# Performance work log

Measured on AMD Instinct MI355X. Metric: run time of the kernel, lower is better.

Reference implementation:

```python
import jax, jax.numpy as jnp
import numpy as np

N = 50000
E = 640000
IN_DIM = 23
HID = 128
NUM_CLASS = 12


def setup_inputs() -> dict:
    key = jax.random.key(0)
    ks = jax.random.split(key, 12)
    x = jax.random.normal(ks[0], (N, IN_DIM), dtype=jnp.float32)
    edge_index = jax.random.randint(ks[1], (2, E), 0, N, dtype=jnp.int32)

    def glorot(k, shape):
        fan_in, fan_out = shape
        lim = np.sqrt(6.0 / (fan_in + fan_out)).astype(np.float32)
        return jax.random.uniform(k, shape, jnp.float32, -lim, lim)

    W1 = glorot(ks[2], (IN_DIM, HID)); b1 = jnp.zeros((HID,), jnp.float32)
    W2 = glorot(ks[3], (HID, HID));    b2 = jnp.zeros((HID,), jnp.float32)
    W3 = glorot(ks[4], (HID, HID));    b3 = jnp.zeros((HID,), jnp.float32)
    Wc1 = glorot(ks[5], (HID, 64));    bc1 = jnp.zeros((64,), jnp.float32)
    Wc2 = glorot(ks[6], (64, NUM_CLASS)); bc2 = jnp.zeros((NUM_CLASS,), jnp.float32)
    return {"x": x, "edge_index": edge_index,
            "W1": W1, "b1": b1, "W2": W2, "b2": b2, "W3": W3, "b3": b3,
            "Wc1": Wc1, "bc1": bc1, "Wc2": Wc2, "bc2": bc2}


def _gcn_norm(edge_index, n_nodes):
    # add self loops, compute symmetric normalization D^-1/2 (A+I) D^-1/2
    loop = jnp.arange(n_nodes, dtype=edge_index.dtype)
    src = jnp.concatenate([edge_index[0], loop])
    dst = jnp.concatenate([edge_index[1], loop])
    deg = jax.ops.segment_sum(jnp.ones_like(dst, dtype=jnp.float32), dst,
                              num_segments=n_nodes)
    dinv = jax.lax.rsqrt(deg)  # deg >= 1 due to self loops
    norm = dinv[src] * dinv[dst]  # [E + N]
    return src, dst, norm


def _gcn_layer(h, W, b, src, dst, norm, n_nodes):
    h = h @ W                          # linear (bias applied after aggregation, per PyG)
    msg = h[src] * norm[:, None]       # gather + scale
    out = jax.ops.segment_sum(msg, dst, num_segments=n_nodes)  # scatter-add
    return out + b


def reference(x, edge_index, W1, b1, W2, b2, W3, b3, Wc1, bc1, Wc2, bc2):
    n = x.shape[0]
    src, dst, norm = _gcn_norm(edge_index, n)
    h = jnp.tanh(_gcn_layer(x, W1, b1, src, dst, norm, n))
    h = jnp.tanh(_gcn_layer(h, W2, b2, src, dst, norm, n))
    h = jnp.tanh(_gcn_layer(h, W3, b3, src, dst, norm, n))
    # dropout is identity in eval mode
    out = h @ Wc1 + bc1
    out = out @ Wc2 + bc2
    return out
```

## Files before the change

### kernel.cpp

```cpp
#include <hip/hip_runtime.h>
#include <math.h>

#define NN 50000
#define EE 640000
#define IND 23
#define HID 128
#define MIDD 64
#define NCLS 12
#define NB 49
#define QS 32766.0f
#define INVQS (1.0f / 32766.0f)

typedef short short8v __attribute__((ext_vector_type(8)));
typedef float f32x4 __attribute__((ext_vector_type(4)));

__device__ __forceinline__ short f2bf(float f) {
    unsigned u = __float_as_uint(f);
    unsigned r = (u + 0x7FFFu + ((u >> 16) & 1u)) >> 16;
    return (short)r;
}
__device__ __forceinline__ float bf2f(short s) {
    return __uint_as_float(((unsigned)(unsigned short)s) << 16);
}

__global__ __launch_bounds__(256) void k_pre(const int* __restrict__ dst,
                                             int* __restrict__ cnt,
                                             const float* __restrict__ Wc1,
                                             const float* __restrict__ bc1,
                                             const float* __restrict__ Wc2,
                                             const float* __restrict__ bc2,
                                             float* __restrict__ Wcc,
                                             float* __restrict__ bcc,
                                             const float* __restrict__ W2,
                                             const float* __restrict__ W3,
                                             short* __restrict__ w2hi,
                                             short* __restrict__ w2lo,
                                             short* __restrict__ w3hi,
                                             short* __restrict__ w3lo) {
    const int bid = blockIdx.x;
    const int tid = threadIdx.x;
    if (bid < 2500) {
        int i = bid * 256 + tid;
        if (i < EE) atomicAdd(&cnt[dst[i]], 1);
        return;
    }
    if (bid < 2506) {
        int t = (bid - 2500) * 256 + tid;
        if (t < HID * NCLS) {
            int k = t / NCLS, c = t % NCLS;
            float s = 0.f;
#pragma unroll 8
            for (int j = 0; j < MIDD; ++j) s += Wc1[k * MIDD + j] * Wc2[j * NCLS + c];
            Wcc[t] = s;
        }
        if (t < NCLS) {
            float s = bc2[t];
#pragma unroll 8
            for (int j = 0; j < MIDD; ++j) s += bc1[j] * Wc2[j * NCLS + t];
            bcc[t] = s;
        }
        return;
    }
    int bb = bid - 2506;
    const float* W = (bb < 64) ? W2 : W3;
    short* hi = (bb < 64) ? w2hi : w3hi;
    short* lo = (bb < 64) ? w2lo : w3lo;
    int i = (bb & 63) * 256 + tid;
    int k = i >> 7, c = i & 127;
    float w = W[i];
    short h = f2bf(w);
    short l = f2bf(w - bf2f(h));
    int t = k >> 5, g = (k >> 3) & 3, j = k & 7;
    hi[((t * 4 + g) * 128 + c) * 8 + j] = h;
    lo[((t * 4 + g) * 128 + c) * 8 + j] = l;
}

__global__ __launch_bounds__(256) void k_scan_local(const int* __restrict__ cnt,
                                                    int* __restrict__ row_ptr,
                                                    float* __restrict__ dinv,
                                                    int* __restrict__ sums) {
    __shared__ int wtot[4];
    const int tid = threadIdx.x;
    const int wid = tid >> 6, lane = tid & 63;
    const int base = blockIdx.x * 1024 + tid * 4;
    int v[4];
#pragma unroll
    for (int t = 0; t < 4; ++t) {
        int i = base + t;
        v[t] = (i < NN) ? cnt[i] : 0;
        if (i < NN) dinv[i] = rsqrtf((float)v[t] + 1.0f);
    }
    int slocal = v[0] + v[1] + v[2] + v[3];
    int val = slocal;
#pragma unroll
    for (int off = 1; off < 64; off <<= 1) {
        int t = __shfl_up(val, off, 64);
        if (lane >= off) val += t;
    }
    if (lane == 63) wtot[wid] = val;
    __syncthreads();
    int woff = 0;
#pragma unroll
    for (int w = 0; w < 4; ++w) woff += (w < wid) ? wtot[w] : 0;
    int run = woff + val - slocal;
#pragma unroll
    for (int t = 0; t < 4; ++t) {
        int i = base + t;
        if (i < NN) row_ptr[i] = run;
        run += v[t];
    }
    if (tid == 255) sums[blockIdx.x] = woff + val;
}

__global__ __launch_bounds__(256) void k_scan_apply2(int* __restrict__ row_ptr,
                                                     const int* __restrict__ sums,
                                                     int* __restrict__ cursor) {
    __shared__ int so;
    const int tid = threadIdx.x;
    if (tid < 64) {
        int a = (tid < (int)blockIdx.x) ? sums[tid] : 0;
        int b = (tid < NB) ? sums[tid] : 0;
#pragma unroll
        for (int off = 32; off; off >>= 1) {
            a += __shfl_down(a, off, 64);
            b += __shfl_down(b, off, 64);
        }
        if (tid == 0) {
            so = a;
            if (blockIdx.x == NB - 1) row_ptr[NN] = b;
        }
    }
    __syncthreads();
    const int o = so;
    const int base = blockIdx.x * 1024 + tid * 4;
#pragma unroll
    for (int t = 0; t < 4; ++t) {
        int i = base + t;
        if (i < NN) {
            int rp = row_ptr[i] + o;
            row_ptr[i] = rp;
            cursor[i] = rp;
        }
    }
}

__global__ __launch_bounds__(256) void k_fillpad(const int* __restrict__ src,
                                                 const int* __restrict__ dst,
                                                 int* __restrict__ cursor,
                                                 const float* __restrict__ dinv,
                                                 int2* __restrict__ e_sn,
                                                 const float* __restrict__ x,
                                                 float* __restrict__ xp) {
    const int bid = blockIdx.x;
    const int tid = threadIdx.x;
    if (bid < 2500) {
        int i = bid * 256 + tid;
        if (i < EE) {
            int s = src[i];
            int d = dst[i];
            float w = dinv[s];
            int pos = atomicAdd(&cursor[d], 1);
            e_sn[pos] = make_int2(s, __float_as_int(w));
        }
        return;
    }
    int i = (bid - 2500) * 256 + tid;
    int node = i >> 5, f = i & 31;
    xp[i] = (f < IND) ? x[node * IND + f] * dinv[node] : 0.f;
}

__global__ __launch_bounds__(256) void k_l1(const float* __restrict__ xp,
                                            const float* __restrict__ W1,
                                            const float* __restrict__ b1,
                                            const int* __restrict__ row_ptr,
                                            const int2* __restrict__ e_sn,
                                            const float* __restrict__ dinv,
                                            short* __restrict__ outq) {
    const int tid = threadIdx.x;
    const int i = blockIdx.x * 4 + (tid >> 6);
    const int lane = tid & 63;
    const int slot = lane >> 3;
    const int f = lane & 7;
    const float4* xp4 = (const float4*)xp;
    const int beg = row_ptr[i];
    const int deg = row_ptr[i + 1] - beg;
    float4 acc = make_float4(0.f, 0.f, 0.f, 0.f);
    for (int base = 0; base < deg; base += 64) {
        const int cnt = min(64, deg - base);
        int s_l = 0;
        if (lane < cnt) s_l = e_sn[beg + base + lane].x;
        int e = 0;
        for (; e + 8 <= cnt; e += 8) {
            int s = __shfl(s_l, e + slot, 64);
            float4 v = xp4[s * 8 + f];
            acc.x += v.x; acc.y += v.y; acc.z += v.z; acc.w += v.w;
        }
        if (e < cnt) {
            int s = __shfl(s_l, e + slot, 64);
            if (e + slot < cnt) {
                float4 v = xp4[s * 8 + f];
                acc.x += v.x; acc.y += v.y; acc.z += v.z; acc.w += v.w;
            }
        }
    }
#pragma unroll
    for (int off = 32; off >= 8; off >>= 1) {
        acc.x += __shfl_down(acc.x, off, 64);
        acc.y += __shfl_down(acc.y, off, 64);
        acc.z += __shfl_down(acc.z, off, 64);
        acc.w += __shfl_down(acc.w, off, 64);
    }
    const float di = dinv[i];
    if (lane < 8) {
        float4 v = xp4[i * 8 + lane];
        acc.x = (acc.x + v.x) * di; acc.y = (acc.y + v.y) * di;
        acc.z = (acc.z + v.z) * di; acc.w = (acc.w + v.w) * di;
    }
    float a0 = b1[lane], a1 = b1[lane + 64];
#pragma unroll
    for (int k = 0; k < IND; ++k) {
        float comp = ((k & 3) == 0) ? acc.x : ((k & 3) == 1) ? acc.y
                   : ((k & 3) == 2) ? acc.z : acc.w;
        float xk = __shfl(comp, k >> 2, 64);
        a0 += xk * W1[k * HID + lane];
        a1 += xk * W1[k * HID + lane + 64];
    }
    outq[i * HID + lane]      = (short)__float2int_rn(tanhf(a0) * QS);
    outq[i * HID + lane + 64] = (short)__float2int_rn(tanhf(a1) * QS);
}

__global__ __launch_bounds__(256) void k_aggq(const short* __restrict__ hq,
                                              const int* __restrict__ row_ptr,
                                              const int2* __restrict__ e_sn,
                                              const float* __restrict__ dinv,
                                              float* __restrict__ aggf) {
    const int tid = threadIdx.x;
    const int i = blockIdx.x * 4 + (tid >> 6);
    const int lane = tid & 63;
    const int slot = lane >> 4;
    const int f = lane & 15;
    const short8v* h8 = (const short8v*)hq;
    const int beg = row_ptr[i];
    const int deg = row_ptr[i + 1] - beg;
    float facc[8];
#pragma unroll
    for (int t = 0; t < 8; ++t) facc[t] = 0.f;
    for (int base = 0; base < deg; base += 64) {
        const int cnt = min(64, deg - base);
        int s_l = 0; float n_l = 0.f;
        if (lane < cnt) {
            int2 sn = e_sn[beg + base + lane];
            s_l = sn.x;
            n_l = __int_as_float(sn.y);
        }
        int e = 0;
#pragma unroll 4
        for (; e + 4 <= cnt; e += 4) {
            int s = __shfl(s_l, e + slot, 64);
            float nr = __shfl(n_l, e + slot, 64);
            short8v v = h8[s * 16 + f];
#pragma unroll
            for (int t = 0; t < 8; ++t) facc[t] += (float)v[t] * nr;
        }
        if (e < cnt) {
            int s = __shfl(s_l, e + slot, 64);
            float nr = __shfl(n_l, e + slot, 64);
            if (e + slot < cnt) {
                short8v v = h8[s * 16 + f];
#pragma unroll
                for (int t = 0; t < 8; ++t) facc[t] += (float)v[t] * nr;
            }
        }
    }
#pragma unroll
    for (int off = 32; off >= 16; off >>= 1)
#pragma unroll
        for (int t = 0; t < 8; ++t) facc[t] += __shfl_down(facc[t], off, 64);
    if (lane < 16) {
        const float di = dinv[i];
        const float sc = di * INVQS;
        short8v v = h8[i * 16 + lane];
        float4 o0, o1;
        o0.x = (facc[0] + di * (float)v[0]) * sc;
        o0.y = (facc[1] + di * (float)v[1]) * sc;
        o0.z = (facc[2] + di * (float)v[2]) * sc;
        o0.w = (facc[3] + di * (float)v[3]) * sc;
        o1.x = (facc[4] + di * (float)v[4]) * sc;
        o1.y = (facc[5] + di * (float)v[5]) * sc;
        o1.z = (facc[6] + di * (float)v[6]) * sc;
        o1.w = (facc[7] + di * (float)v[7]) * sc;
        ((float4*)aggf)[i * 32 + lane * 2]     = o0;
        ((float4*)aggf)[i * 32 + lane * 2 + 1] = o1;
    }
}

__device__ __forceinline__ void gemm_core(const float* __restrict__ hin,
                                          const short8v* __restrict__ whi8,
                                          const short8v* __restrict__ wlo8,
                                          int row, bool rv, int g, int c16,
                                          f32x4 acc[8]) {
#pragma unroll
    for (int t = 0; t < 4; ++t) {
        float4 a0 = make_float4(0.f, 0.f, 0.f, 0.f), a1 = a0;
        if (rv) {
            const float4* hp = (const float4*)&hin[row * HID + t * 32 + g * 8];
            a0 = hp[0]; a1 = hp[1];
        }
        float av[8];
        av[0] = a0.x; av[1] = a0.y; av[2] = a0.z; av[3] = a0.w;
        av[4] = a1.x; av[5] = a1.y; av[6] = a1.z; av[7] = a1.w;
        short8v ahi, alo;
#pragma unroll
        for (int j = 0; j < 8; ++j) {
            short h = f2bf(av[j]);
            ahi[j] = h;
            alo[j] = f2bf(av[j] - bf2f(h));
        }
        const int wb = (t * 4 + g) * 128 + c16;
#pragma unroll
        for (int n = 0; n < 8; ++n) {
            short8v bh = whi8[wb + n * 16];
            short8v bl = wlo8[wb + n * 16];
            acc[n] = __builtin_amdgcn_mfma_f32_16x16x32_bf16(ahi, bh, acc[n], 0, 0, 0);
            acc[n] = __builtin_amdgcn_mfma_f32_16x16x32_bf16(ahi, bl, acc[n], 0, 0, 0);
            acc[n] = __builtin_amdgcn_mfma_f32_16x16x32_bf16(alo, bh, acc[n], 0, 0, 0);
        }
    }
}

__global__ __launch_bounds__(256) void k_gemm_q(const float* __restrict__ hin,
                                                const short* __restrict__ whi,
                                                const short* __restrict__ wlo,
                                                const float* __restrict__ bias,
                                                short* __restrict__ qout) {
    const int tid = threadIdx.x;
    const int lane = tid & 63, w = tid >> 6;
    const int g = lane >> 4, c16 = lane & 15;
    const int rbase = blockIdx.x * 64 + w * 16;
    f32x4 acc[8];
#pragma unroll
    for (int n = 0; n < 8; ++n) acc[n] = f32x4{0.f, 0.f, 0.f, 0.f};
    gemm_core(hin, (const short8v*)whi, (const short8v*)wlo,
              rbase + c16, (rbase + c16) < NN, g, c16, acc);
#pragma unroll
    for (int n = 0; n < 8; ++n) {
        const float bb = bias[n * 16 + c16];
#pragma unroll
        for (int r = 0; r < 4; ++r) {
            int nd = rbase + 4 * g + r;
            if (nd < NN) {
                float v = tanhf(acc[n][r] + bb);
                qout[nd * HID + n * 16 + c16] = (short)__float2int_rn(v * QS);
            }
        }
    }
}

__global__ __launch_bounds__(256) void k_gemm_head(const float* __restrict__ hin,
                                                   const short* __restrict__ whi,
                                                   const short* __restrict__ wlo,
                                                   const float* __restrict__ bias,
                                                   const float* __restrict__ Wcc,
                                                   const float* __restrict__ bcc,
                                                   float* __restrict__ outp) {
    __shared__ float WccS[HID * NCLS + 16];
    const int tid = threadIdx.x;
    const int lane = tid & 63, w = tid >> 6;
    const int g = lane >> 4, c16 = lane & 15;
    const int rbase = blockIdx.x * 64 + w * 16;
    for (int t = tid; t < HID * NCLS; t += 256) WccS[t] = Wcc[t];
    if (tid < NCLS) WccS[HID * NCLS + tid] = bcc[tid];
    __syncthreads();
    f32x4 acc[8];
#pragma unroll
    for (int n = 0; n < 8; ++n) acc[n] = f32x4{0.f, 0.f, 0.f, 0.f};
    gemm_core(hin, (const short8v*)whi, (const short8v*)wlo,
              rbase + c16, (rbase + c16) < NN, g, c16, acc);
    float part[4][12];
#pragma unroll
    for (int r = 0; r < 4; ++r)
#pragma unroll
        for (int c = 0; c < 12; ++c) part[r][c] = 0.f;
#pragma unroll
    for (int n = 0; n < 8; ++n) {
        const float bb = bias[n * 16 + c16];
        const float4* wr = (const float4*)&WccS[(n * 16 + c16) * NCLS];
        float4 wa = wr[0], wb = wr[1], wc = wr[2];
#pragma unroll
        for (int r = 0; r < 4; ++r) {
            float v = tanhf(acc[n][r] + bb);
            part[r][0]  += v * wa.x; part[r][1]  += v * wa.y;
            part[r][2]  += v * wa.z; part[r][3]  += v * wa.w;
            part[r][4]  += v * wb.x; part[r][5]  += v * wb.y;
            part[r][6]  += v * wb.z; part[r][7]  += v * wb.w;
            part[r][8]  += v * wc.x; part[r][9]  += v * wc.y;
            part[r][10] += v * wc.z; part[r][11] += v * wc.w;
        }
    }
#pragma unroll
    for (int off = 8; off; off >>= 1)
#pragma unroll
        for (int r = 0; r < 4; ++r)
#pragma unroll
            for (int c = 0; c < 12; ++c)
                part[r][c] += __shfl_down(part[r][c], off, 64);
    if (c16 == 0) {
#pragma unroll
        for (int r = 0; r < 4; ++r) {
            int nd = rbase + 4 * g + r;
            if (nd < NN) {
                float4* op = (float4*)&outp[nd * NCLS];
                op[0] = make_float4(part[r][0] + WccS[HID * NCLS + 0],
                                    part[r][1] + WccS[HID * NCLS + 1],
                                    part[r][2] + WccS[HID * NCLS + 2],
                                    part[r][3] + WccS[HID * NCLS + 3]);
                op[1] = make_float4(part[r][4] + WccS[HID * NCLS + 4],
                                    part[r][5] + WccS[HID * NCLS + 5],
                                    part[r][6] + WccS[HID * NCLS + 6],
                                    part[r][7] + WccS[HID * NCLS + 7]);
                op[2] = make_float4(part[r][8] + WccS[HID * NCLS + 8],
                                    part[r][9] + WccS[HID * NCLS + 9],
                                    part[r][10] + WccS[HID * NCLS + 10],
                                    part[r][11] + WccS[HID * NCLS + 11]);
            }
        }
    }
}


extern "C" void kernel_launch(void* const* d_in, const int* in_sizes, int n_in,
                              void* d_out, int out_size, void* d_ws, size_t ws_size,
                              hipStream_t stream) {
    const float* x    = (const float*)d_in[0];
    const int*   edge = (const int*)d_in[1];
    const int*   src  = edge;
    const int*   dst  = edge + EE;
    const float* W1  = (const float*)d_in[2];  const float* b1  = (const float*)d_in[3];
    const float* W2  = (const float*)d_in[4];  const float* b2  = (const float*)d_in[5];
    const float* W3  = (const float*)d_in[6];  const float* b3  = (const float*)d_in[7];
    const float* Wc1 = (const float*)d_in[8];  const float* bc1 = (const float*)d_in[9];
    const float* Wc2 = (const float*)d_in[10]; const float* bc2 = (const float*)d_in[11];
    float* outp = (float*)d_out;

    char* p = (char*)d_ws;
    int*   cnt     = (int*)p;   p += 200064;
    int*   row_ptr = (int*)p;   p += 200064;
    float* dinv    = (float*)p; p += 200064;
    int*   sums    = (int*)p;   p += 256;
    int2*  e_sn    = (int2*)p;  p += (size_t)EE * 8;
    float* xp      = (float*)p; p += (size_t)NN * 32 * 4;
    short* q       = (short*)p; p += (size_t)NN * HID * 2;
    float* aggf    = (float*)p; p += (size_t)NN * HID * 4;
    float* Wcc     = (float*)p; p += HID * NCLS * 4;
    float* bcc     = (float*)p; p += 256;
    short* w2hi    = (short*)p; p += 32768;
    short* w2lo    = (short*)p; p += 32768;
    short* w3hi    = (short*)p; p += 32768;
    short* w3lo    = (short*)p; p += 32768;

    hipMemsetAsync(cnt, 0, (size_t)NN * 4, stream);
    k_pre        <<<2634, 256, 0, stream>>>(dst, cnt, Wc1, bc1, Wc2, bc2, Wcc, bcc,
                                            W2, W3, w2hi, w2lo, w3hi, w3lo);
    k_scan_local <<<NB, 256, 0, stream>>>(cnt, row_ptr, dinv, sums);
    k_scan_apply2<<<NB, 256, 0, stream>>>(row_ptr, sums, cnt);
    k_fillpad    <<<8750, 256, 0, stream>>>(src, dst, cnt, dinv, e_sn, x, xp);

    k_l1  <<<NN / 4, 256, 0, stream>>>(xp, W1, b1, row_ptr, e_sn, dinv, q);
    k_aggq     <<<NN / 4, 256, 0, stream>>>(q, row_ptr, e_sn, dinv, aggf);
    k_gemm_q   <<<(NN + 63) / 64, 256, 0, stream>>>(aggf, w2hi, w2lo, b2, q);
    k_aggq     <<<NN / 4, 256, 0, stream>>>(q, row_ptr, e_sn, dinv, aggf);
    k_gemm_head<<<(NN + 63) / 64, 256, 0, stream>>>(aggf, w3hi, w3lo, b3, Wcc, bcc, outp);
}
```

Baseline: 300.5 us.

## Build CSR via two-pass bucketed partition and local sort instead of global atomics

Replaces the per-edge global atomic cursor scatter into CSR with a two-level counting sort. Edges are first partitioned into buckets of 128 destination nodes, using block-local histograms and one global atomic per bucket. A second kernel then sorts each bucket in shared memory and writes it out coalesced. This aims to cut contended global atomics and scattered writes, at the cost of an extra kernel, extra intermediate buffers and deterministic-order changes within rows.

```diff
diff --git a/kernel.cpp b/kernel.cpp
--- a/kernel.cpp
+++ b/kernel.cpp
@@ -10,9 +10,15 @@
 #define NB 49
 #define QS 32766.0f
 #define INVQS (1.0f / 32766.0f)
+#define BSH 7
+#define NBK 391
+#define CHUNK 4096
+#define NPB 157
+#define PADB 6250
 
 typedef short short8v __attribute__((ext_vector_type(8)));
 typedef float f32x4 __attribute__((ext_vector_type(4)));
+typedef unsigned long long u64;
 
 __device__ __forceinline__ short f2bf(float f) {
     unsigned u = __float_as_uint(f);
@@ -114,7 +120,7 @@
 
 __global__ __launch_bounds__(256) void k_scan_apply2(int* __restrict__ row_ptr,
                                                      const int* __restrict__ sums,
-                                                     int* __restrict__ cursor) {
+                                                     int* __restrict__ bcurA) {
     __shared__ int so;
     const int tid = threadIdx.x;
     if (tid < 64) {
@@ -139,34 +145,113 @@
         if (i < NN) {
             int rp = row_ptr[i] + o;
             row_ptr[i] = rp;
-            cursor[i] = rp;
-        }
-    }
-}
-
-__global__ __launch_bounds__(256) void k_fillpad(const int* __restrict__ src,
-                                                 const int* __restrict__ dst,
-                                                 int* __restrict__ cursor,
-                                                 const float* __restrict__ dinv,
-                                                 int2* __restrict__ e_sn,
-                                                 const float* __restrict__ x,
-                                                 float* __restrict__ xp) {
+            if ((i & 127) == 0) bcurA[i >> BSH] = rp;
+        }
+    }
+}
+
+__global__ __launch_bounds__(256) void k_part(const int* __restrict__ src,
+                                              const int* __restrict__ dst,
+                                              const float* __restrict__ dinv,
+                                              int* __restrict__ bcurA,
+                                              u64* __restrict__ sw_g,
+                                              int* __restrict__ d_g,
+                                              const float* __restrict__ x,
+                                              float* __restrict__ xp) {
     const int bid = blockIdx.x;
     const int tid = threadIdx.x;
-    if (bid < 2500) {
-        int i = bid * 256 + tid;
+    if (bid >= NPB) {
+        int i = (bid - NPB) * 256 + tid;
+        int node = i >> 5, f = i & 31;
+        xp[i] = (f < IND) ? x[node * IND + f] * dinv[node] : 0.f;
+        return;
+    }
+    __shared__ int hist[NBK], base[NBK], cur[NBK], gb[NBK];
+    __shared__ u64 lsw[CHUNK];
+    __shared__ int ld[CHUNK];
+    const int e0 = bid * CHUNK;
+    const int total = min(CHUNK, EE - e0);
+    for (int t = tid; t < NBK; t += 256) hist[t] = 0;
+    __syncthreads();
+    int sv[16], dv[16];
+#pragma unroll
+    for (int t = 0; t < 16; ++t) {
+        int i = e0 + t * 256 + tid;
         if (i < EE) {
-            int s = src[i];
-            int d = dst[i];
-            float w = dinv[s];
-            int pos = atomicAdd(&cursor[d], 1);
-            e_sn[pos] = make_int2(s, __float_as_int(w));
-        }
-        return;
-    }
-    int i = (bid - 2500) * 256 + tid;
-    int node = i >> 5, f = i & 31;
-    xp[i] = (f < IND) ? x[node * IND + f] * dinv[node] : 0.f;
+            sv[t] = src[i];
+            dv[t] = dst[i];
+            atomicAdd(&hist[dv[t] >> BSH], 1);
+        } else dv[t] = -1;
+    }
+    __syncthreads();
+    if (tid < 64) {
+        int carry = 0;
+        for (int c = 0; c < NBK; c += 64) {
+            int idx = c + tid;
+            int v = (idx < NBK) ? hist[idx] : 0;
+            int sc = v;
+#pragma unroll
+            for (int off = 1; off < 64; off <<= 1) {
+                int tv = __shfl_up(sc, off, 64);
+                if (tid >= off) sc += tv;
+            }
+            if (idx < NBK) base[idx] = carry + sc - v;
+            carry += __shfl(sc, 63, 64);
+        }
+    }
+    __syncthreads();
+    for (int t = tid; t < NBK; t += 256) {
+        cur[t] = base[t];
+        gb[t] = hist[t] ? atomicAdd(&bcurA[t], hist[t]) : 0;
+    }
+    __syncthreads();
+#pragma unroll
+    for (int t = 0; t < 16; ++t) {
+        if (dv[t] >= 0) {
+            int b = dv[t] >> BSH;
+            int r = atomicAdd(&cur[b], 1);
+            lsw[r] = (unsigned)sv[t] |
+                     ((u64)__float_as_uint(dinv[sv[t]]) << 32);
+            ld[r] = dv[t];
+        }
+    }
+    __syncthreads();
+    for (int j = tid; j < total; j += 256) {
+        int d = ld[j];
+        int b = d >> BSH;
+        int gpos = gb[b] + (j - base[b]);
+        sw_g[gpos] = lsw[j];
+        d_g[gpos] = d;
+    }
+}
+
+__global__ __launch_bounds__(256) void k_sort(const int* __restrict__ row_ptr,
+                                              const u64* __restrict__ sw_g,
+                                              const int* __restrict__ d_g,
+                                              u64* __restrict__ e_sn) {
+    __shared__ int rloc[129];
+    __shared__ int curl[128];
+    __shared__ u64 osw[3072];
+    const int bid = blockIdx.x, tid = threadIdx.x;
+    const int n0 = bid << BSH;
+    const int nlast = min(128, NN - n0);
+    if (tid <= nlast) rloc[tid] = row_ptr[n0 + tid];
+    if (tid < 128) curl[tid] = 0;
+    __syncthreads();
+    const int rbeg = rloc[0];
+    const int cnt = rloc[nlast] - rbeg;
+    for (int j = tid; j < cnt; j += 256) {
+        int d = d_g[rbeg + j];
+        int li = d - n0;
+        int r = atomicAdd(&curl[li], 1);
+        int pl = (rloc[li] - rbeg) + r;
+        u64 v = sw_g[rbeg + j];
+        if (pl < 3072) osw[pl] = v;
+        else e_sn[rbeg + pl] = v;
+    }
+    __syncthreads();
+    const int lim = min(cnt, 3072);
+    for (int j = tid; j < lim; j += 256) e_sn[rbeg + j] = osw[j];
 }
 
 __global__ __launch_bounds__(256) void k_l1(const float* __restrict__ xp,
@@ -447,7 +532,10 @@
     int*   row_ptr = (int*)p;   p += 200064;
     float* dinv    = (float*)p; p += 200064;
     int*   sums    = (int*)p;   p += 256;
+    int*   bcurA   = (int*)p;   p += 2048;
     int2*  e_sn    = (int2*)p;  p += (size_t)EE * 8;
+    u64*   sw_g    = (u64*)p;   p += (size_t)EE * 8;
+    int*   d_g     = (int*)p;   p += (size_t)EE * 4;
     float* xp      = (float*)p; p += (size_t)NN * 32 * 4;
     short* q       = (short*)p; p += (size_t)NN * HID * 2;
     float* aggf    = (float*)p; p += (size_t)NN * HID * 4;
@@ -462,8 +550,10 @@
     k_pre        <<<2634, 256, 0, stream>>>(dst, cnt, Wc1, bc1, Wc2, bc2, Wcc, bcc,
                                             W2, W3, w2hi, w2lo, w3hi, w3lo);
     k_scan_local <<<NB, 256, 0, stream>>>(cnt, row_ptr, dinv, sums);
-    k_scan_apply2<<<NB, 256, 0, stream>>>(row_ptr, sums, cnt);
-    k_fillpad    <<<8750, 256, 0, stream>>>(src, dst, cnt, dinv, e_sn, x, xp);
+    k_scan_apply2<<<NB, 256, 0, stream>>>(row_ptr, sums, bcurA);
+    k_part       <<<NPB + PADB, 256, 0, stream>>>(src, dst, dinv, bcurA,
+                                                  sw_g, d_g, x, xp);
+    k_sort       <<<NBK, 256, 0, stream>>>(row_ptr, sw_g, d_g, (u64*)e_sn);
 
     k_l1  <<<NN / 4, 256, 0, stream>>>(xp, W1, b1, row_ptr, e_sn, dinv, q);
     k_aggq     <<<NN / 4, 256, 0, stream>>>(q, row_ptr, e_sn, dinv, aggf);
```

New measurement: 284.8 us. -5.2%, faster.
